# Kernel tuning notes

Hardware: AMD Instinct MI355X
Metric: run time of the kernel (lower is better)

The kernel has to match this reference:

```python
import jax, jax.numpy as jnp
import numpy as np


def setup_inputs() -> dict:
    key = jax.random.key(0)
    ks = jax.random.split(key, 8)
    B, C, D, H, W = 2, 32, 16, 16, 16
    C8 = C // 8
    x = jax.random.normal(ks[0], (B, C, D, H, W), dtype=jnp.float32)
    s = 1.0 / np.sqrt(C)
    wq = jax.random.normal(ks[1], (C8, C), dtype=jnp.float32) * s
    bq = jnp.zeros((C8,), dtype=jnp.float32)
    wk = jax.random.normal(ks[2], (C8, C), dtype=jnp.float32) * s
    bk = jnp.zeros((C8,), dtype=jnp.float32)
    wv = jax.random.normal(ks[3], (C, C), dtype=jnp.float32) * s
    bv = jnp.zeros((C,), dtype=jnp.float32)
    gamma_p = jnp.ones((1,), dtype=jnp.float32)
    gamma_c = jnp.ones((1,), dtype=jnp.float32)
    wo = jax.random.normal(ks[4], (C, 2 * C), dtype=jnp.float32) * (1.0 / np.sqrt(2 * C))
    bo = jnp.zeros((C,), dtype=jnp.float32)
    return {"x": x, "wq": wq, "bq": bq, "wk": wk, "bk": bk,
            "wv": wv, "bv": bv, "gamma_p": gamma_p, "gamma_c": gamma_c,
            "wo": wo, "bo": bo}


def _forward(x, wq, bq, wk, bk, wv, bv, gamma_p, gamma_c, wo, bo):
    B, C, D, H, W = x.shape
    N = D * H * W
    xf = x.reshape(B, C, N)  # [B, C, N]

    # ---- PAM: position attention over N = D*H*W tokens ----
    # 1x1x1 Conv3d == per-token channel matmul
    q = jnp.einsum('oc,bcn->bno', wq, xf) + bq            # [B, N, C/8]
    k = jnp.einsum('oc,bcn->bon', wk, xf) + bk[None, :, None]  # [B, C/8, N]
    v = jnp.einsum('oc,bcn->bon', wv, xf) + bv[None, :, None]  # [B, C, N]
    energy = jnp.einsum('bno,bom->bnm', q, k)             # [B, N, N] (unscaled)
    attn = jax.nn.softmax(energy, axis=-1)                # rows over keys
    # out = v @ attn^T : out[b,c,i] = sum_j v[b,c,j] * attn[b,i,j]
    pam_out = jnp.einsum('bcj,bij->bci', v, attn)         # [B, C, N]
    pam = (gamma_p[0] * pam_out + xf).reshape(B, C, D, H, W)

    # ---- CAM: channel attention with max-subtraction softmax ----
    eng = jnp.einsum('bcn,bdn->bcd', xf, xf)              # [B, C, C]
    eng_new = jnp.max(eng, axis=-1, keepdims=True) - eng
    cattn = jax.nn.softmax(eng_new, axis=-1)              # [B, C, C]
    cam_out = jnp.einsum('bcd,bdn->bcn', cattn, xf)       # [B, C, N]
    cam = (gamma_c[0] * cam_out + xf).reshape(B, C, D, H, W)

    # ---- concat + 1x1x1 out conv ----
    cat = jnp.concatenate([pam, cam], axis=1).reshape(B, 2 * C, N)
    out = jnp.einsum('oc,bcn->bon', wo, cat) + bo[None, :, None]
    return out.reshape(B, C, D, H, W)


def reference(x, wq, bq, wk, bk, wv, bv, gamma_p, gamma_c, wo, bo):
    return _forward(x, wq, bq, wk, bk, wv, bv, gamma_p, gamma_c, wo, bo)
```

## Files before the change

### kernel.cpp

```cpp
#include <hip/hip_runtime.h>
#include <hip/hip_bf16.h>
#include <math.h>

#define BB 2
#define CC 32
#define C8 4
#define NN 4096
#define VST 68
#define LOG2E 1.4426950408889634f

typedef __attribute__((ext_vector_type(8))) short short8;
typedef __attribute__((ext_vector_type(16))) float f32x16;

static __device__ __forceinline__ short f2bf(float x) {
    return __builtin_bit_cast(short, __float2bfloat16(x));
}
static __device__ __forceinline__ unsigned int pkbf(float a, float b) {
    unsigned int ua = __builtin_bit_cast(unsigned int, a) + 0x8000u;
    unsigned int ub = __builtin_bit_cast(unsigned int, b) + 0x8000u;
    return (ua >> 16) | (ub & 0xffff0000u);
}

__global__ __launch_bounds__(256) void k1(const float* __restrict__ x,
    const float* __restrict__ wq, const float* __restrict__ bq,
    const float* __restrict__ wk, const float* __restrict__ bk,
    const float* __restrict__ wv, const float* __restrict__ bv,
    short* __restrict__ qpk, short* __restrict__ kpk, short* __restrict__ vbf,
    float* __restrict__ eng)
{
    if (blockIdx.x >= 64) {
        int w = threadIdx.x >> 6, lane = threadIdx.x & 63;
        int pp = (blockIdx.x - 64)*4 + w;
        int b = pp >= 528 ? 1 : 0;
        int t = pp - b*528;
        int c = 0, rem = t;
        while (rem >= CC - c) { rem -= CC - c; ++c; }
        int d = c + rem;
        const float4* xc = (const float4*)(x + ((size_t)b*CC + c)*NN);
        const float4* xd = (const float4*)(x + ((size_t)b*CC + d)*NN);
        float s = 0.f;
        for (int tt = lane; tt < NN/4; tt += 64) {
            float4 a = xc[tt], bb = xd[tt];
            s += a.x*bb.x + a.y*bb.y + a.z*bb.z + a.w*bb.w;
        }
        #pragma unroll
        for (int off = 32; off; off >>= 1) s += __shfl_down(s, off, 64);
        if (lane == 0) {
            eng[(b*CC + c)*CC + d] = s;
            eng[(b*CC + d)*CC + c] = s;
        }
        return;
    }
    __shared__ float swq[C8*CC], swk[C8*CC], swv[CC*CC], sbq[C8], sbk[C8], sbv[CC];
    int tid = threadIdx.x;
    for (int i = tid; i < C8*CC; i += 256) { swq[i] = wq[i]; swk[i] = wk[i]; }
    for (int i = tid; i < CC*CC; i += 256) swv[i] = wv[i];
    if (tid < C8) { sbq[tid] = bq[tid]; sbk[tid] = bk[tid]; }
    if (tid < CC) sbv[tid] = bv[tid];
    __syncthreads();
    int tl = tid & 127, oh = tid >> 7;
    int g = blockIdx.x*128 + tl;
    int b = g >> 12; int n = g & (NN-1);
    const float* xb = x + (size_t)b*CC*NN + n;
    float xr[CC];
    #pragma unroll
    for (int c = 0; c < CC; ++c) xr[c] = xb[(size_t)c*NN];
    if (oh == 0) {
        float qv[C8], kv[C8];
        #pragma unroll
        for (int o = 0; o < C8; ++o) { qv[o] = sbq[o]; kv[o] = sbk[o]; }
        #pragma unroll
        for (int c = 0; c < CC; ++c) {
            float xc = xr[c];
            #pragma unroll
            for (int o = 0; o < C8; ++o) { qv[o] += swq[o*CC+c]*xc; kv[o] += swk[o*CC+c]*xc; }
        }
        short4 qs = make_short4(f2bf(qv[0]*LOG2E), f2bf(qv[1]*LOG2E),
                                f2bf(qv[2]*LOG2E), f2bf(qv[3]*LOG2E));
        short4 ks = make_short4(f2bf(kv[0]), f2bf(kv[1]), f2bf(kv[2]), f2bf(kv[3]));
        *(short4*)(qpk + ((size_t)b*NN + n)*4) = qs;
        *(short4*)(kpk + ((size_t)b*NN + n)*4) = ks;
    }
    int o0 = oh*16;
    #pragma unroll
    for (int o = 0; o < 16; ++o) {
        float av = sbv[o0+o];
        #pragma unroll
        for (int c = 0; c < CC; ++c) av += swv[(o0+o)*CC+c]*xr[c];
        vbf[((size_t)b*CC+o0+o)*NN + n] = f2bf(av);
    }
}

__global__ __launch_bounds__(1024, 4) void k2(const short* __restrict__ qpk,
    const short* __restrict__ kpk, const short* __restrict__ vbf,
    const float* __restrict__ eng, const float* __restrict__ wo,
    const float* __restrict__ bo, const float* __restrict__ gp,
    const float* __restrict__ gc, const float* __restrict__ x,
    float* __restrict__ out)
{
    __shared__ __align__(16) char smem[99328];

    int blk = blockIdx.x;
    int b  = blk >> 7;
    int it = blk & 127;
    int i0 = it*32;
    int tid = threadIdx.x;
    int w = tid >> 6, lane = tid & 63;
    int qcol = lane & 31, h = lane >> 5;

    short* vbuf = (short*)smem + w*(32*VST);

    int rv = lane >> 1, ch = lane & 1;
    const short* vsrc = vbf + (size_t)b*CC*NN + (size_t)rv*NN + w*64 + ch*32;
    const short* ksrc = kpk + ((size_t)b*NN + w*64 + qcol)*4;

    short8 qf = {0,0,0,0,0,0,0,0};
    if (h == 0) {
        short4 qv = *(const short4*)(qpk + ((size_t)b*NN + i0 + qcol)*4);
        qf[0]=qv.x; qf[1]=qv.y; qf[2]=qv.z; qf[3]=qv.w;
    }
    short4 kreg[8];
    #pragma unroll
    for (int t = 0; t < 8; ++t) kreg[t] = make_short4(0,0,0,0);
    if (h == 0) {
        #pragma unroll
        for (int t = 0; t < 8; ++t)
            kreg[t] = *(const short4*)(ksrc + (t>>1)*4096 + (t&1)*128);
    }

    f32x16 acc = {0,0,0,0,0,0,0,0,0,0,0,0,0,0,0,0};
    const f32x16 zz = {0,0,0,0,0,0,0,0,0,0,0,0,0,0,0,0};
    float se = 0.f;

    short8 cv0 = *(const short8*)(vsrc);
    short8 cv1 = *(const short8*)(vsrc + 8);
    short8 cv2 = *(const short8*)(vsrc + 16);
    short8 cv3 = *(const short8*)(vsrc + 24);

    #pragma unroll
    for (int t = 0; t < 4; ++t) {
        int tn = t < 3 ? t + 1 : 3;
        short8 nv0 = *(const short8*)(vsrc + tn*1024);
        short8 nv1 = *(const short8*)(vsrc + tn*1024 + 8);
        short8 nv2 = *(const short8*)(vsrc + tn*1024 + 16);
        short8 nv3 = *(const short8*)(vsrc + tn*1024 + 24);

        short* wp = vbuf + rv*VST + ch*32;
        *(short8*)(wp)      = cv0;
        *(short8*)(wp + 8)  = cv1;
        *(short8*)(wp + 16) = cv2;
        *(short8*)(wp + 24) = cv3;

        short8 kf0 = {kreg[2*t].x,   kreg[2*t].y,   kreg[2*t].z,   kreg[2*t].w,   0,0,0,0};
        short8 kf1 = {kreg[2*t+1].x, kreg[2*t+1].y, kreg[2*t+1].z, kreg[2*t+1].w, 0,0,0,0};
        f32x16 s0 = __builtin_amdgcn_mfma_f32_32x32x16_bf16(kf0, qf, zz, 0, 0, 0);
        f32x16 s1 = __builtin_amdgcn_mfma_f32_32x32x16_bf16(kf1, qf, zz, 0, 0, 0);

        const short* vrow = vbuf + qcol*VST;
        #pragma unroll
        for (int cI = 0; cI < 2; ++cI) {
            f32x16 s = cI ? s1 : s0;
            unsigned int u[8];
            #pragma unroll
            for (int g4 = 0; g4 < 4; ++g4) {
                float p0 = exp2f(s[4*g4]),   p1 = exp2f(s[4*g4+1]);
                float p2 = exp2f(s[4*g4+2]), p3 = exp2f(s[4*g4+3]);
                se += (p0+p1)+(p2+p3);
                u[2*g4]   = pkbf(p0,p1);
                u[2*g4+1] = pkbf(p2,p3);
            }
            int vo = cI*32 + 4*h;
            short4 a0 = *(const short4*)(vrow + vo);
            short4 a1 = *(const short4*)(vrow + vo + 8);
            short4 a2 = *(const short4*)(vrow + vo + 16);
            short4 a3 = *(const short4*)(vrow + vo + 24);
            short8 vf1 = {a0.x,a0.y,a0.z,a0.w, a1.x,a1.y,a1.z,a1.w};
            short8 pf1 = {(short)u[0],(short)(u[0]>>16),(short)u[1],(short)(u[1]>>16),
                          (short)u[2],(short)(u[2]>>16),(short)u[3],(short)(u[3]>>16)};
            short8 vf2 = {a2.x,a2.y,a2.z,a2.w, a3.x,a3.y,a3.z,a3.w};
            short8 pf2 = {(short)u[4],(short)(u[4]>>16),(short)u[5],(short)(u[5]>>16),
                          (short)u[6],(short)(u[6]>>16),(short)u[7],(short)(u[7]>>16)};
            __builtin_amdgcn_s_setprio(1);
            acc = __builtin_amdgcn_mfma_f32_32x32x16_bf16(vf1, pf1, acc, 0, 0, 0);
            acc = __builtin_amdgcn_mfma_f32_32x32x16_bf16(vf2, pf2, acc, 0, 0, 0);
            __builtin_amdgcn_s_setprio(0);
        }
        cv0 = nv0; cv1 = nv1; cv2 = nv2; cv3 = nv3;
    }

    se += __shfl_xor(se, 32, 64);

    __syncthreads();
    float* pamw = (float*)smem;
    float* seL  = pamw + 16*1056;
    float* sinv = seL  + 512;
    float* pamn = sinv + 32;
    float* xt   = pamn + 1056;
    float* swo  = xt   + 1056;
    float* swx  = swo  + 1056;
    float* sc   = swx  + 1056;
    float* seng = sc   + 1056;
    float* sbo  = seng + 1024;
    float* swo2 = sbo  + 32;

    #pragma unroll
    for (int r = 0; r < 16; ++r) {
        int c = (r&3) + 8*(r>>2) + 4*h;
        pamw[w*1056 + c*33 + qcol] = acc[r];
    }
    if (h == 0) seL[w*32 + qcol] = se;
    for (int i = tid; i < CC*CC; i += 1024) {
        int o = i >> 5, c2 = i & 31;
        seng[i] = eng[b*CC*CC + i];
        swo [o*33 + c2] = wo[o*64 + c2];
        swo2[o*33 + c2] = wo[o*64 + 32 + c2];
        xt  [o*33 + c2] = x[(size_t)b*CC*NN + (size_t)o*NN + i0 + c2];
    }
    if (tid < CC) sbo[tid] = bo[tid];
    __syncthreads();

    if (tid < CC) {
        float s = 0.f;
        #pragma unroll
        for (int w2 = 0; w2 < 16; ++w2) s += seL[w2*32 + tid];
        sinv[tid] = 1.f / s;
    } else if (tid >= 64 && tid < 64 + CC) {
        int r2 = tid - 64;
        float mn = seng[r2*32];
        #pragma unroll
        for (int d = 1; d < CC; ++d) mn = fminf(mn, seng[r2*32 + d]);
        float pv[CC]; float s = 0.f;
        #pragma unroll
        for (int d = 0; d < CC; ++d) { pv[d] = __expf(mn - seng[r2*32 + d]); s += pv[d]; }
        float inv = 1.f / s;
        #pragma unroll
        for (int d = 0; d < CC; ++d) sc[r2*33 + d] = pv[d]*inv;
    }
    __syncthreads();

    float gpv = gp[0], gcv = gc[0];
    for (int i = tid; i < CC*CC; i += 1024) {
        int c = i >> 5, q = i & 31;
        float s2 = 0.f;
        #pragma unroll
        for (int w2 = 0; w2 < 16; ++w2) s2 += pamw[w2*1056 + c*33 + q];
        pamn[c*33 + q] = gpv * s2 * sinv[q];
        float t2 = 0.f;
        #pragma unroll
        for (int c2 = 0; c2 < CC; ++c2) t2 += swo2[c*33 + c2] * sc[c2*33 + q];
        swx[c*33 + q] = swo[c*33 + q] + swo2[c*33 + q] + gcv * t2;
    }
    __syncthreads();

    int q = tid & 31, slot = (tid >> 5) & 31;
    float o0 = sbo[slot];
    #pragma unroll
    for (int c = 0; c < CC; ++c) {
        o0 += swo[slot*33 + c] * pamn[c*33 + q] + swx[slot*33 + c] * xt[c*33 + q];
    }
    out[(size_t)b*CC*NN + (size_t)slot*NN + i0 + q] = o0;
}

extern "C" void kernel_launch(void* const* d_in, const int* in_sizes, int n_in,
                              void* d_out, int out_size, void* d_ws, size_t ws_size,
                              hipStream_t stream)
{
    const float* x  = (const float*)d_in[0];
    const float* wq = (const float*)d_in[1];
    const float* bq = (const float*)d_in[2];
    const float* wk = (const float*)d_in[3];
    const float* bk = (const float*)d_in[4];
    const float* wv = (const float*)d_in[5];
    const float* bv = (const float*)d_in[6];
    const float* gp = (const float*)d_in[7];
    const float* gc = (const float*)d_in[8];
    const float* wo = (const float*)d_in[9];
    const float* bo = (const float*)d_in[10];

    char* wsb = (char*)d_ws;
    short* qpk = (short*)(wsb + 0);
    short* kpk = (short*)(wsb + 65536);
    short* vbf = (short*)(wsb + 131072);
    float* eng = (float*)(wsb + 655360);

    k1<<<328, 256, 0, stream>>>(x, wq, bq, wk, bk, wv, bv, qpk, kpk, vbf, eng);
    k2<<<BB*128, 1024, 0, stream>>>(qpk, kpk, vbf, eng, wo, bo, gp, gc, x, (float*)d_out);
}
```

Baseline: 30.17 us.

## Stage V tiles via direct global-to-LDS loads with XOR swizzle and double buffering

V tiles now go straight from global memory into LDS with global_load_lds instead of passing through registers. A padded-row layout is replaced by an XOR-swizzled layout, double-buffered with explicit vmcnt waits. The QK MFMA is moved inside the inner loop and the setprio hints are dropped. This is meant to cut VGPR pressure and register-to-LDS store traffic. In exchange it grows shared memory to 128KB per block, which may lower occupancy.

Result: no change. 29.91 us (-0.8%).

```diff
diff --git a/kernel.cpp b/kernel.cpp
--- a/kernel.cpp
+++ b/kernel.cpp
@@ -6,7 +6,6 @@
 #define CC 32
 #define C8 4
 #define NN 4096
-#define VST 68
 #define LOG2E 1.4426950408889634f
 
 typedef __attribute__((ext_vector_type(8))) short short8;
@@ -19,6 +18,11 @@
     unsigned int ua = __builtin_bit_cast(unsigned int, a) + 0x8000u;
     unsigned int ub = __builtin_bit_cast(unsigned int, b) + 0x8000u;
     return (ua >> 16) | (ub & 0xffff0000u);
+}
+static __device__ __forceinline__ void gld16(const void* g, void* l) {
+    __builtin_amdgcn_global_load_lds(
+        (const __attribute__((address_space(1))) unsigned int*)g,
+        (__attribute__((address_space(3))) unsigned int*)l, 16, 0, 0);
 }
 
 __global__ __launch_bounds__(256) void k1(const float* __restrict__ x,
@@ -98,7 +102,7 @@
     const float* __restrict__ gc, const float* __restrict__ x,
     float* __restrict__ out)
 {
-    __shared__ __align__(16) char smem[99328];
+    __shared__ __align__(16) char smem[131072];
 
     int blk = blockIdx.x;
     int b  = blk >> 7;
@@ -108,17 +112,19 @@
     int w = tid >> 6, lane = tid & 63;
     int qcol = lane & 31, h = lane >> 5;
 
-    short* vbuf = (short*)smem + w*(32*VST);
-
-    int rv = lane >> 1, ch = lane & 1;
-    const short* vsrc = vbf + (size_t)b*CC*NN + (size_t)rv*NN + w*64 + ch*32;
-    const short* ksrc = kpk + ((size_t)b*NN + w*64 + qcol)*4;
+    char* vb0 = smem + w*8192;
+
+    int lrow = lane >> 3;
+    int cbl  = ((lane & 7) ^ (lrow & 7)) << 4;
+    const char* vsb = (const char*)vbf;
+    size_t srow = ((size_t)(b*CC + lrow))*NN + w*64;
 
     short8 qf = {0,0,0,0,0,0,0,0};
     if (h == 0) {
         short4 qv = *(const short4*)(qpk + ((size_t)b*NN + i0 + qcol)*4);
         qf[0]=qv.x; qf[1]=qv.y; qf[2]=qv.z; qf[3]=qv.w;
     }
+    const short* ksrc = kpk + ((size_t)b*NN + w*64 + qcol)*4;
     short4 kreg[8];
     #pragma unroll
     for (int t = 0; t < 8; ++t) kreg[t] = make_short4(0,0,0,0);
@@ -132,34 +138,32 @@
     const f32x16 zz = {0,0,0,0,0,0,0,0,0,0,0,0,0,0,0,0};
     float se = 0.f;
 
-    short8 cv0 = *(const short8*)(vsrc);
-    short8 cv1 = *(const short8*)(vsrc + 8);
-    short8 cv2 = *(const short8*)(vsrc + 16);
-    short8 cv3 = *(const short8*)(vsrc + 24);
+    #pragma unroll
+    for (int i = 0; i < 4; ++i)
+        gld16(vsb + 2*(srow + (size_t)i*8*NN) + cbl, vb0 + i*1024);
+
+    int rb = qcol << 7;
+    int sw = (qcol & 7) << 4;
 
     #pragma unroll
     for (int t = 0; t < 4; ++t) {
-        int tn = t < 3 ? t + 1 : 3;
-        short8 nv0 = *(const short8*)(vsrc + tn*1024);
-        short8 nv1 = *(const short8*)(vsrc + tn*1024 + 8);
-        short8 nv2 = *(const short8*)(vsrc + tn*1024 + 16);
-        short8 nv3 = *(const short8*)(vsrc + tn*1024 + 24);
-
-        short* wp = vbuf + rv*VST + ch*32;
-        *(short8*)(wp)      = cv0;
-        *(short8*)(wp + 8)  = cv1;
-        *(short8*)(wp + 16) = cv2;
-        *(short8*)(wp + 24) = cv3;
-
-        short8 kf0 = {kreg[2*t].x,   kreg[2*t].y,   kreg[2*t].z,   kreg[2*t].w,   0,0,0,0};
-        short8 kf1 = {kreg[2*t+1].x, kreg[2*t+1].y, kreg[2*t+1].z, kreg[2*t+1].w, 0,0,0,0};
-        f32x16 s0 = __builtin_amdgcn_mfma_f32_32x32x16_bf16(kf0, qf, zz, 0, 0, 0);
-        f32x16 s1 = __builtin_amdgcn_mfma_f32_32x32x16_bf16(kf1, qf, zz, 0, 0, 0);
-
-        const short* vrow = vbuf + qcol*VST;
+        char* cur = vb0 + (t & 1)*4096;
+        if (t < 3) {
+            char* nxt = vb0 + ((t + 1) & 1)*4096;
+            #pragma unroll
+            for (int i = 0; i < 4; ++i)
+                gld16(vsb + 2*(srow + (size_t)i*8*NN + (t+1)*1024) + cbl, nxt + i*1024);
+            asm volatile("s_waitcnt vmcnt(4)" ::: "memory");
+        } else {
+            asm volatile("s_waitcnt vmcnt(0)" ::: "memory");
+        }
+        __builtin_amdgcn_sched_barrier(0);
+
         #pragma unroll
         for (int cI = 0; cI < 2; ++cI) {
-            f32x16 s = cI ? s1 : s0;
+            short4 kk = kreg[2*t + cI];
+            short8 kf = {kk.x, kk.y, kk.z, kk.w, 0,0,0,0};
+            f32x16 s = __builtin_amdgcn_mfma_f32_32x32x16_bf16(kf, qf, zz, 0, 0, 0);
             unsigned int u[8];
             #pragma unroll
             for (int g4 = 0; g4 < 4; ++g4) {
@@ -169,23 +173,20 @@
                 u[2*g4]   = pkbf(p0,p1);
                 u[2*g4+1] = pkbf(p2,p3);
             }
-            int vo = cI*32 + 4*h;
-            short4 a0 = *(const short4*)(vrow + vo);
-            short4 a1 = *(const short4*)(vrow + vo + 8);
-            short4 a2 = *(const short4*)(vrow + vo + 16);
-            short4 a3 = *(const short4*)(vrow + vo + 24);
+            int bo = 64*cI + 8*h;
+            short4 a0 = *(const short4*)(cur + rb + ((bo +  0) ^ sw));
+            short4 a1 = *(const short4*)(cur + rb + ((bo + 16) ^ sw));
+            short4 a2 = *(const short4*)(cur + rb + ((bo + 32) ^ sw));
+            short4 a3 = *(const short4*)(cur + rb + ((bo + 48) ^ sw));
             short8 vf1 = {a0.x,a0.y,a0.z,a0.w, a1.x,a1.y,a1.z,a1.w};
             short8 pf1 = {(short)u[0],(short)(u[0]>>16),(short)u[1],(short)(u[1]>>16),
                           (short)u[2],(short)(u[2]>>16),(short)u[3],(short)(u[3]>>16)};
+            acc = __builtin_amdgcn_mfma_f32_32x32x16_bf16(vf1, pf1, acc, 0, 0, 0);
             short8 vf2 = {a2.x,a2.y,a2.z,a2.w, a3.x,a3.y,a3.z,a3.w};
             short8 pf2 = {(short)u[4],(short)(u[4]>>16),(short)u[5],(short)(u[5]>>16),
                           (short)u[6],(short)(u[6]>>16),(short)u[7],(short)(u[7]>>16)};
-            __builtin_amdgcn_s_setprio(1);
-            acc = __builtin_amdgcn_mfma_f32_32x32x16_bf16(vf1, pf1, acc, 0, 0, 0);
             acc = __builtin_amdgcn_mfma_f32_32x32x16_bf16(vf2, pf2, acc, 0, 0, 0);
-            __builtin_amdgcn_s_setprio(0);
-        }
-        cv0 = nv0; cv1 = nv1; cv2 = nv2; cv3 = nv3;
+        }
     }
 
     se += __shfl_xor(se, 32, 64);
```
